# Performance work log

Measured on AMD Instinct MI355X. Metric: run time of the kernel, lower is better.

The kernel has to match this reference:

```python
import jax, jax.numpy as jnp
import numpy as np

N, B, CIN = 2048, 16, 1
M = 4096
COUT = 64
R = 128


def setup_inputs() -> dict:
    key = jax.random.key(0)
    k1, k2, k3, k4, k5 = jax.random.split(key, 5)
    return {
        "context_in": jax.random.normal(k1, (N, B, CIN), dtype=jnp.float32),
        "context_out": jax.random.normal(k2, (N, B, COUT), dtype=jnp.float32),
        "target_in": jax.random.normal(k3, (M, B, CIN), dtype=jnp.float32),
        "lengthscale": jnp.ones((1,), dtype=jnp.float32),
        "W": jax.random.normal(k4, (R, COUT + 1), dtype=jnp.float32),
        "b": jax.random.normal(k5, (R,), dtype=jnp.float32),
    }


def reference(context_in, context_out, target_in, lengthscale, W, b):
    # context_in: (N,B,Cin), context_out: (N,B,Cout), target_in: (M,B,Cin)
    n, batch, _ = context_in.shape
    # density channel prepended -> (N,B,Cout+1)
    dens = jnp.ones((n, batch, 1), dtype=context_in.dtype)
    co = jnp.concatenate([dens, context_out], axis=-1)
    ci = jnp.transpose(context_in, (1, 0, 2))   # (B,N,Cin)
    ti = jnp.transpose(target_in, (1, 0, 2))    # (B,M,Cin)
    # squared pairwise distances (B,N,M)
    d2 = (jnp.sum(ci * ci, -1)[:, :, None]
          + jnp.sum(ti * ti, -1)[:, None, :]
          - 2.0 * jnp.einsum('bnd,bmd->bnm', ci, ti))
    d2 = jnp.maximum(d2, 0.0)
    # RBF kernel: exp(-0.5 * d2 / lengthscale^2)
    K = jnp.exp(-0.5 * d2 / (lengthscale[0] ** 2))  # (B,N,M)
    # weighted sum over context points: (B,M,Cout+1)
    out = jnp.einsum('nbc,bnm->bmc', co, K)
    # density normalization of non-density channels
    out = jnp.concatenate([out[..., :1], out[..., 1:] / (out[..., :1] + 1e-8)], axis=-1)
    # linear projection (Cout+1 -> R)
    out = out @ W.T + b
    return jnp.transpose(out, (1, 0, 2))  # (M,B,R)
```

## Files before the change

kernel.cpp:

```cpp
#include <hip/hip_runtime.h>
#include <hip/hip_bf16.h>


#define N_CTX 2048
#define BATCH 16
#define M_TGT 4096
#define COUT  64
#define RDIM  128

#define WS_CO_BYTES (N_CTX * BATCH * COUT * 2)
#define WS_SX_OFF   WS_CO_BYTES
#define WS_WT_OFF   (WS_SX_OFF + N_CTX * BATCH * 4)

#define SSCALE 0.8493222f

typedef __attribute__((ext_vector_type(8)))  short        bf16x8;
typedef __attribute__((ext_vector_type(4)))  float        floatx4;
typedef __attribute__((ext_vector_type(4)))  unsigned int uint4v;

#if __has_builtin(__builtin_amdgcn_exp2f)
#define EXP2F __builtin_amdgcn_exp2f
#else
#define EXP2F exp2f
#endif

static __device__ __forceinline__ unsigned int pack_bf16(float lo, float hi) {
    __hip_bfloat162 h = __float22bfloat162_rn(make_float2(lo, hi));
    return *reinterpret_cast<unsigned int*>(&h);
}
static __device__ __forceinline__ unsigned short f2bf(float f) {
    __hip_bfloat16 h = __float2bfloat16(f);
    return *reinterpret_cast<unsigned short*>(&h);
}

__global__ __launch_bounds__(256)
void convdeepset_prep(const float* __restrict__ ci, const float* __restrict__ co,
                      const float* __restrict__ ls, const float* __restrict__ W,
                      unsigned char* __restrict__ ws)
{
    unsigned short* cow = (unsigned short*)ws;
    float*          sx  = (float*)(ws + WS_SX_OFF);
    unsigned short* wt  = (unsigned short*)(ws + WS_WT_OFF);
    const int blk = blockIdx.x, tid = threadIdx.x;

    if (blk < 1024) {
#pragma unroll
        for (int it = 0; it < 4; ++it) {
            const int f  = (it * 1024 + blk) * 256 + tid;
            const int c  = f & 63;
            const int bb = (f >> 6) & 15;
            const int n  = (f >> 10) * 2;
            const float f0 = co[((size_t)n       * BATCH + bb) * COUT + c];
            const float f1 = co[((size_t)(n + 1) * BATCH + bb) * COUT + c];
            *(unsigned int*)&cow[bb * 131072 + (n >> 3) * 512 + c * 8 + (n & 7)]
                = pack_bf16(f0, f1);
        }
    } else if (blk < 1152) {
        const int f = (blk - 1024) * 256 + tid;
        const int n = f & 2047, bb = f >> 11;
        const float s = SSCALE / ls[0];
        sx[bb * 2048 + n] = s * ci[(size_t)n * BATCH + bb];
    } else {
        for (int f = tid; f < 8192; f += 256) {
            const int cp = f & 7, r = (f >> 3) & 127, ch = f >> 10;
            wt[ch * 1024 + r * 8 + cp] = f2bf(W[r * 65 + 1 + ch * 8 + cp]);
        }
    }
}

__global__ __launch_bounds__(256)
void convdeepset_main(const float* __restrict__ ti, const float* __restrict__ ls,
                      const float* __restrict__ W,  const float* __restrict__ bias,
                      const unsigned char* __restrict__ ws, float* __restrict__ out)
{
    __shared__ float sxt[N_CTX];
    __shared__ unsigned short vstage[4][1024];
    __shared__ float w0l[RDIM], biasl[RDIM];

    const int tid  = threadIdx.x;
    const int lane = tid & 63;
    const int wv   = tid >> 6;
    const int g2   = lane >> 4;
    const int l15  = lane & 15;
    const int b    = blockIdx.x >> 6;
    const int mt   = blockIdx.x & 63;
    const int m0   = mt * 64 + wv * 16;

    const float4* sxg = (const float4*)(ws + WS_SX_OFF) + b * (N_CTX / 4);
    float4* s4 = (float4*)sxt;
    s4[tid]       = sxg[tid];
    s4[tid + 256] = sxg[tid + 256];
    if (tid < RDIM) { w0l[tid] = W[tid * 65]; biasl[tid] = bias[tid]; }

    const float s  = SSCALE / ls[0];
    const float sy = s * ti[(size_t)(m0 + l15) * BATCH + b];
    __syncthreads();

    const unsigned short* cowB = (const unsigned short*)ws
                               + (size_t)b * 131072 + g2 * 512 + l15 * 8;

    floatx4 acc[4];
#pragma unroll
    for (int q = 0; q < 4; ++q)
#pragma unroll
        for (int i = 0; i < 4; ++i) acc[q][i] = 0.0f;
    float dp0 = 0.0f, dp1 = 0.0f;

    bf16x8 A0, A1, A2, A3, B0, B1, B2, B3;
    float4 Axa, Axb, Bxa, Bxb;
    {
        const unsigned short* p = cowB;
        A0 = *(const bf16x8*)(p);       A1 = *(const bf16x8*)(p + 128);
        A2 = *(const bf16x8*)(p + 256); A3 = *(const bf16x8*)(p + 384);
        Axa = *(const float4*)&sxt[g2 * 8]; Axb = *(const float4*)&sxt[g2 * 8 + 4];
        p = cowB + 2048;
        B0 = *(const bf16x8*)(p);       B1 = *(const bf16x8*)(p + 128);
        B2 = *(const bf16x8*)(p + 256); B3 = *(const bf16x8*)(p + 384);
        Bxa = *(const float4*)&sxt[32 + g2 * 8]; Bxb = *(const float4*)&sxt[32 + g2 * 8 + 4];
    }

    auto kstep = [&](bf16x8& b0, bf16x8& b1, bf16x8& b2, bf16x8& b3,
                     float4& xa, float4& xb, int kpre) {
        const bf16x8 c0 = b0, c1 = b1, c2 = b2, c3 = b3;
        const float4 ca = xa, cb = xb;
        const unsigned short* p = cowB + kpre * 2048;
        b0 = *(const bf16x8*)(p);       b1 = *(const bf16x8*)(p + 128);
        b2 = *(const bf16x8*)(p + 256); b3 = *(const bf16x8*)(p + 384);
        const float* xp = &sxt[kpre * 32 + g2 * 8];
        xa = *(const float4*)(xp); xb = *(const float4*)(xp + 4);
        const float x0 = ca.x, x1 = ca.y, x2 = ca.z, x3 = ca.w;
        const float x4 = cb.x, x5 = cb.y, x6 = cb.z, x7 = cb.w;
        float kv[8];
        {
            float t;
            t = x0 - sy; kv[0] = EXP2F(-(t * t));
            t = x1 - sy; kv[1] = EXP2F(-(t * t));
            t = x2 - sy; kv[2] = EXP2F(-(t * t));
            t = x3 - sy; kv[3] = EXP2F(-(t * t));
            t = x4 - sy; kv[4] = EXP2F(-(t * t));
            t = x5 - sy; kv[5] = EXP2F(-(t * t));
            t = x6 - sy; kv[6] = EXP2F(-(t * t));
            t = x7 - sy; kv[7] = EXP2F(-(t * t));
        }
        dp0 += (kv[0] + kv[1]) + (kv[2] + kv[3]);
        dp1 += (kv[4] + kv[5]) + (kv[6] + kv[7]);
        uint4v aw;
#pragma unroll
        for (int q2 = 0; q2 < 4; ++q2) aw[q2] = pack_bf16(kv[2 * q2], kv[2 * q2 + 1]);
        const bf16x8 av = __builtin_bit_cast(bf16x8, aw);
        acc[0] = __builtin_amdgcn_mfma_f32_16x16x32_bf16(av, c0, acc[0], 0, 0, 0);
        acc[1] = __builtin_amdgcn_mfma_f32_16x16x32_bf16(av, c1, acc[1], 0, 0, 0);
        acc[2] = __builtin_amdgcn_mfma_f32_16x16x32_bf16(av, c2, acc[2], 0, 0, 0);
        acc[3] = __builtin_amdgcn_mfma_f32_16x16x32_bf16(av, c3, acc[3], 0, 0, 0);
    };

    for (int ks = 0; ks < 64; ks += 2) {
        kstep(A0, A1, A2, A3, Axa, Axb, (ks + 2 < 64) ? ks + 2 : 63);
        kstep(B0, B1, B2, B3, Bxa, Bxb, (ks + 3 < 64) ? ks + 3 : 63);
    }

    float dens = dp0 + dp1;
    dens += __shfl_xor(dens, 16);
    dens += __shfl_xor(dens, 32);

    float drow[4];
    unsigned short* vs = vstage[wv];
#pragma unroll
    for (int reg = 0; reg < 4; ++reg) {
        const int m = (lane >> 4) * 4 + reg;
        const float dr = __shfl(dens, m);
        drow[reg] = dr;
        const float dinv = 1.0f / (dr + 1e-8f);
#pragma unroll
        for (int q = 0; q < 4; ++q) {
            const int c = q * 16 + l15;
            vs[(c >> 3) * 128 + m * 8 + (c & 7)] = f2bf(acc[q][reg] * dinv);
        }
    }

    const unsigned short* wtg = (const unsigned short*)(ws + WS_WT_OFF);
    floatx4 pacc[8];
#pragma unroll
    for (int rt = 0; rt < 8; ++rt)
#pragma unroll
        for (int i = 0; i < 4; ++i) pacc[rt][i] = 0.0f;

#pragma unroll
    for (int s2 = 0; s2 < 2; ++s2) {
        const int ch = s2 * 4 + g2;
        const bf16x8 avp = *(const bf16x8*)&vs[ch * 128 + l15 * 8];
#pragma unroll
        for (int rt = 0; rt < 8; ++rt) {
            const bf16x8 bvp = *(const bf16x8*)&wtg[ch * 1024 + (rt * 16 + l15) * 8];
            pacc[rt] = __builtin_amdgcn_mfma_f32_16x16x32_bf16(avp, bvp, pacc[rt], 0, 0, 0);
        }
    }

#pragma unroll
    for (int rt = 0; rt < 8; ++rt) {
        const int r = rt * 16 + l15;
        const float w0v = w0l[r];
        const float bv  = biasl[r];
#pragma unroll
        for (int reg = 0; reg < 4; ++reg) {
            const int m = (lane >> 4) * 4 + reg;
            out[((size_t)(m0 + m) * BATCH + b) * RDIM + r]
                = pacc[rt][reg] + drow[reg] * w0v + bv;
        }
    }
}

extern "C" void kernel_launch(void* const* d_in, const int* in_sizes, int n_in,
                              void* d_out, int out_size, void* d_ws, size_t ws_size,
                              hipStream_t stream) {
    const float* ci   = (const float*)d_in[0];
    const float* co   = (const float*)d_in[1];
    const float* ti   = (const float*)d_in[2];
    const float* ls   = (const float*)d_in[3];
    const float* W    = (const float*)d_in[4];
    const float* bias = (const float*)d_in[5];
    float* o = (float*)d_out;
    (void)in_sizes; (void)n_in; (void)out_size; (void)ws_size;

    convdeepset_prep<<<1153, 256, 0, stream>>>(ci, co, ls, W, (unsigned char*)d_ws);
    convdeepset_main<<<BATCH * (M_TGT / 64), 256, 0, stream>>>(
        ti, ls, W, bias, (const unsigned char*)d_ws, o);
}
```

Baseline: 124.3 us.

## Split context reduction across waves, MFMA density, XCD-aware mapping, vectorized prep

The main kernel now has each block handle 32 targets instead of 64. Pairs of waves split the 2048 context points, and the second half's partial sums are reduced through shared memory as bf16. The density is accumulated with an extra MFMA against a ones vector rather than scalar adds and shuffles, and normalization moves to after the projection. Blocks are mapped so that each XCD handles two batches, and the software prefetch is replaced by a plain unrolled loop. The prep kernel writes 16-byte vectorized stores. These changes add parallelism and cache locality but double the grid, repeat the sx loads per block, and round the partial sums to bf16.

After: 123.6 us. No clear change (-0.5%).

```diff
diff --git a/kernel.cpp b/kernel.cpp
--- a/kernel.cpp
+++ b/kernel.cpp
@@ -44,17 +44,19 @@
     const int blk = blockIdx.x, tid = threadIdx.x;
 
     if (blk < 1024) {
-#pragma unroll
-        for (int it = 0; it < 4; ++it) {
-            const int f  = (it * 1024 + blk) * 256 + tid;
-            const int c  = f & 63;
-            const int bb = (f >> 6) & 15;
-            const int n  = (f >> 10) * 2;
-            const float f0 = co[((size_t)n       * BATCH + bb) * COUT + c];
-            const float f1 = co[((size_t)(n + 1) * BATCH + bb) * COUT + c];
-            *(unsigned int*)&cow[bb * 131072 + (n >> 3) * 512 + c * 8 + (n & 7)]
-                = pack_bf16(f0, f1);
-        }
+        const int g    = blk * 4 + (tid >> 6);
+        const int bb   = g & 15;
+        const int nblk = g >> 4;
+        const int c    = tid & 63;
+        const float* rp = co + ((size_t)nblk * 8 * BATCH + bb) * COUT + c;
+        unsigned int u[4];
+#pragma unroll
+        for (int j = 0; j < 4; ++j) {
+            const float f0 = rp[(size_t)(2 * j)     * BATCH * COUT];
+            const float f1 = rp[(size_t)(2 * j + 1) * BATCH * COUT];
+            u[j] = pack_bf16(f0, f1);
+        }
+        *(uint4v*)&cow[(size_t)bb * 131072 + nblk * 512 + c * 8] = *(uint4v*)u;
     } else if (blk < 1152) {
         const int f = (blk - 1024) * 256 + tid;
         const int n = f & 2047, bb = f >> 11;
@@ -68,23 +70,29 @@
     }
 }
 
-__global__ __launch_bounds__(256)
+__global__ __launch_bounds__(256, 7)
 void convdeepset_main(const float* __restrict__ ti, const float* __restrict__ ls,
                       const float* __restrict__ W,  const float* __restrict__ bias,
                       const unsigned char* __restrict__ ws, float* __restrict__ out)
 {
     __shared__ float sxt[N_CTX];
-    __shared__ unsigned short vstage[4][1024];
+    __shared__ unsigned int rbuf[2 * 64 * 12];
+    __shared__ unsigned short vstage[2][1024];
     __shared__ float w0l[RDIM], biasl[RDIM];
 
     const int tid  = threadIdx.x;
     const int lane = tid & 63;
     const int wv   = tid >> 6;
+    const int mh   = wv & 1;
+    const int nh   = wv >> 1;
     const int g2   = lane >> 4;
     const int l15  = lane & 15;
-    const int b    = blockIdx.x >> 6;
-    const int mt   = blockIdx.x & 63;
-    const int m0   = mt * 64 + wv * 16;
+
+    const int xcd = blockIdx.x & 7;
+    const int i   = blockIdx.x >> 3;
+    const int b   = xcd * 2 + (i & 1);
+    const int mt  = i >> 1;
+    const int m0  = mt * 32 + mh * 16;
 
     const float4* sxg = (const float4*)(ws + WS_SX_OFF) + b * (N_CTX / 4);
     float4* s4 = (float4*)sxt;
@@ -96,54 +104,45 @@
     const float sy = s * ti[(size_t)(m0 + l15) * BATCH + b];
     __syncthreads();
 
+    const short onebf = (short)0x3F80;
+    bf16x8 ones;
+#pragma unroll
+    for (int j = 0; j < 8; ++j) ones[j] = onebf;
+
+    const int ks0 = nh * 32;
     const unsigned short* cowB = (const unsigned short*)ws
-                               + (size_t)b * 131072 + g2 * 512 + l15 * 8;
-
-    floatx4 acc[4];
+                               + (size_t)b * 131072 + (ks0 * 4 + g2) * 512 + l15 * 8;
+
+    floatx4 acc[4], accd;
 #pragma unroll
     for (int q = 0; q < 4; ++q)
 #pragma unroll
-        for (int i = 0; i < 4; ++i) acc[q][i] = 0.0f;
-    float dp0 = 0.0f, dp1 = 0.0f;
-
-    bf16x8 A0, A1, A2, A3, B0, B1, B2, B3;
-    float4 Axa, Axb, Bxa, Bxb;
-    {
-        const unsigned short* p = cowB;
-        A0 = *(const bf16x8*)(p);       A1 = *(const bf16x8*)(p + 128);
-        A2 = *(const bf16x8*)(p + 256); A3 = *(const bf16x8*)(p + 384);
-        Axa = *(const float4*)&sxt[g2 * 8]; Axb = *(const float4*)&sxt[g2 * 8 + 4];
-        p = cowB + 2048;
-        B0 = *(const bf16x8*)(p);       B1 = *(const bf16x8*)(p + 128);
-        B2 = *(const bf16x8*)(p + 256); B3 = *(const bf16x8*)(p + 384);
-        Bxa = *(const float4*)&sxt[32 + g2 * 8]; Bxb = *(const float4*)&sxt[32 + g2 * 8 + 4];
-    }
-
-    auto kstep = [&](bf16x8& b0, bf16x8& b1, bf16x8& b2, bf16x8& b3,
-                     float4& xa, float4& xb, int kpre) {
-        const bf16x8 c0 = b0, c1 = b1, c2 = b2, c3 = b3;
-        const float4 ca = xa, cb = xb;
-        const unsigned short* p = cowB + kpre * 2048;
-        b0 = *(const bf16x8*)(p);       b1 = *(const bf16x8*)(p + 128);
-        b2 = *(const bf16x8*)(p + 256); b3 = *(const bf16x8*)(p + 384);
-        const float* xp = &sxt[kpre * 32 + g2 * 8];
-        xa = *(const float4*)(xp); xb = *(const float4*)(xp + 4);
-        const float x0 = ca.x, x1 = ca.y, x2 = ca.z, x3 = ca.w;
-        const float x4 = cb.x, x5 = cb.y, x6 = cb.z, x7 = cb.w;
+        for (int e = 0; e < 4; ++e) acc[q][e] = 0.0f;
+#pragma unroll
+    for (int e = 0; e < 4; ++e) accd[e] = 0.0f;
+
+#pragma unroll 2
+    for (int ks = 0; ks < 32; ++ks) {
+        const unsigned short* p = cowB + (size_t)ks * 2048;
+        const bf16x8 c0 = *(const bf16x8*)(p);
+        const bf16x8 c1 = *(const bf16x8*)(p + 128);
+        const bf16x8 c2 = *(const bf16x8*)(p + 256);
+        const bf16x8 c3 = *(const bf16x8*)(p + 384);
+        const float* xp = &sxt[(ks0 + ks) * 32 + g2 * 8];
+        const float4 xa = *(const float4*)(xp);
+        const float4 xb = *(const float4*)(xp + 4);
         float kv[8];
         {
             float t;
-            t = x0 - sy; kv[0] = EXP2F(-(t * t));
-            t = x1 - sy; kv[1] = EXP2F(-(t * t));
-            t = x2 - sy; kv[2] = EXP2F(-(t * t));
-            t = x3 - sy; kv[3] = EXP2F(-(t * t));
-            t = x4 - sy; kv[4] = EXP2F(-(t * t));
-            t = x5 - sy; kv[5] = EXP2F(-(t * t));
-            t = x6 - sy; kv[6] = EXP2F(-(t * t));
-            t = x7 - sy; kv[7] = EXP2F(-(t * t));
-        }
-        dp0 += (kv[0] + kv[1]) + (kv[2] + kv[3]);
-        dp1 += (kv[4] + kv[5]) + (kv[6] + kv[7]);
+            t = xa.x - sy; kv[0] = EXP2F(-(t * t));
+            t = xa.y - sy; kv[1] = EXP2F(-(t * t));
+            t = xa.z - sy; kv[2] = EXP2F(-(t * t));
+            t = xa.w - sy; kv[3] = EXP2F(-(t * t));
+            t = xb.x - sy; kv[4] = EXP2F(-(t * t));
+            t = xb.y - sy; kv[5] = EXP2F(-(t * t));
+            t = xb.z - sy; kv[6] = EXP2F(-(t * t));
+            t = xb.w - sy; kv[7] = EXP2F(-(t * t));
+        }
         uint4v aw;
 #pragma unroll
         for (int q2 = 0; q2 < 4; ++q2) aw[q2] = pack_bf16(kv[2 * q2], kv[2 * q2 + 1]);
@@ -152,29 +151,57 @@
         acc[1] = __builtin_amdgcn_mfma_f32_16x16x32_bf16(av, c1, acc[1], 0, 0, 0);
         acc[2] = __builtin_amdgcn_mfma_f32_16x16x32_bf16(av, c2, acc[2], 0, 0, 0);
         acc[3] = __builtin_amdgcn_mfma_f32_16x16x32_bf16(av, c3, acc[3], 0, 0, 0);
-    };
-
-    for (int ks = 0; ks < 64; ks += 2) {
-        kstep(A0, A1, A2, A3, Axa, Axb, (ks + 2 < 64) ? ks + 2 : 63);
-        kstep(B0, B1, B2, B3, Bxa, Bxb, (ks + 3 < 64) ? ks + 3 : 63);
-    }
-
-    float dens = dp0 + dp1;
-    dens += __shfl_xor(dens, 16);
-    dens += __shfl_xor(dens, 32);
-
-    float drow[4];
-    unsigned short* vs = vstage[wv];
+        accd   = __builtin_amdgcn_mfma_f32_16x16x32_bf16(av, ones, accd, 0, 0, 0);
+    }
+
+    if (nh == 1) {
+        unsigned int* slot = &rbuf[(mh * 64 + lane) * 12];
+        unsigned int pu[8];
+#pragma unroll
+        for (int reg = 0; reg < 4; ++reg)
+#pragma unroll
+            for (int qp = 0; qp < 2; ++qp)
+                pu[reg * 2 + qp] = pack_bf16(acc[2 * qp][reg], acc[2 * qp + 1][reg]);
+        *(uint4v*)(slot)     = *(uint4v*)(pu);
+        *(uint4v*)(slot + 4) = *(uint4v*)(pu + 4);
+        *(uint4v*)(slot + 8) = __builtin_bit_cast(uint4v, accd);
+    }
+    __syncthreads();
+    if (nh == 1) return;
+
+    {
+        const unsigned int* slot = &rbuf[(mh * 64 + lane) * 12];
+        const uint4v r0 = *(const uint4v*)(slot);
+        const uint4v r1 = *(const uint4v*)(slot + 4);
+        const floatx4 rd = __builtin_bit_cast(floatx4, *(const uint4v*)(slot + 8));
+#pragma unroll
+        for (int reg = 0; reg < 4; ++reg)
+#pragma unroll
+            for (int qp = 0; qp < 2; ++qp) {
+                const int j = reg * 2 + qp;
+                const unsigned int u = (j < 4) ? r0[j] : r1[j - 4];
+                acc[2 * qp][reg]     += __builtin_bit_cast(float, u << 16);
+                acc[2 * qp + 1][reg] += __builtin_bit_cast(float, u & 0xffff0000u);
+            }
+#pragma unroll
+        for (int e = 0; e < 4; ++e) accd[e] += rd[e];
+    }
+
+    float drow[4], dinv[4];
+#pragma unroll
+    for (int reg = 0; reg < 4; ++reg) {
+        drow[reg] = accd[reg];
+        dinv[reg] = 1.0f / (accd[reg] + 1e-8f);
+    }
+
+    unsigned short* vs = vstage[mh];
 #pragma unroll
     for (int reg = 0; reg < 4; ++reg) {
         const int m = (lane >> 4) * 4 + reg;
-        const float dr = __shfl(dens, m);
-        drow[reg] = dr;
-        const float dinv = 1.0f / (dr + 1e-8f);
 #pragma unroll
         for (int q = 0; q < 4; ++q) {
             const int c = q * 16 + l15;
-            vs[(c >> 3) * 128 + m * 8 + (c & 7)] = f2bf(acc[q][reg] * dinv);
+            vs[(c >> 3) * 128 + m * 8 + (c & 7)] = f2bf(acc[q][reg]);
         }
     }
 
@@ -183,7 +210,7 @@
 #pragma unroll
     for (int rt = 0; rt < 8; ++rt)
 #pragma unroll
-        for (int i = 0; i < 4; ++i) pacc[rt][i] = 0.0f;
+        for (int e = 0; e < 4; ++e) pacc[rt][e] = 0.0f;
 
 #pragma unroll
     for (int s2 = 0; s2 < 2; ++s2) {
@@ -205,7 +232,7 @@
         for (int reg = 0; reg < 4; ++reg) {
             const int m = (lane >> 4) * 4 + reg;
             out[((size_t)(m0 + m) * BATCH + b) * RDIM + r]
-                = pacc[rt][reg] + drow[reg] * w0v + bv;
+                = pacc[rt][reg] * dinv[reg] + drow[reg] * w0v + bv;
         }
     }
 }
@@ -223,6 +250,6 @@
     (void)in_sizes; (void)n_in; (void)out_size; (void)ws_size;
 
     convdeepset_prep<<<1153, 256, 0, stream>>>(ci, co, ls, W, (unsigned char*)d_ws);
-    convdeepset_main<<<BATCH * (M_TGT / 64), 256, 0, stream>>>(
+    convdeepset_main<<<2048, 256, 0, stream>>>(
         ti, ls, W, bias, (const unsigned char*)d_ws, o);
 }
```
